# Performance work log

Measured on AMD Instinct MI355X. Metric: run time of the kernel, lower is better.

The kernel has to match this reference:

```python
import jax, jax.numpy as jnp
import numpy as np

D = 1024
H = 16
DH = D // H  # 64
EPS_LN = 1e-5
CONF_MIN = 1e-6


def sparsemax(z):
    """Sparsemax along the last axis (Martins & Astudillo 2016)."""
    K = z.shape[-1]
    z_sorted = jnp.flip(jnp.sort(z, axis=-1), axis=-1)          # descending
    cssv = jnp.cumsum(z_sorted, axis=-1)                        # cumulative sums
    r = jnp.arange(1, K + 1, dtype=z.dtype)                     # 1..K
    support = (1.0 + r * z_sorted) > cssv                       # bool mask
    k = jnp.sum(support, axis=-1, keepdims=True)                # support size
    tau = (jnp.take_along_axis(cssv, k.astype(jnp.int32) - 1, axis=-1) - 1.0) / k.astype(z.dtype)
    return jnp.maximum(z - tau, 0.0)


def setup_inputs() -> dict:
    key = jax.random.key(0)
    ks = jax.random.split(key, 16)
    B, P, K = 8, 512, 16
    s = 0.02
    return {
        "cell_query": jax.random.normal(ks[0], (B, D), jnp.float32),
        "gene_facets": jax.random.normal(ks[1], (B, P, K, D), jnp.float32),
        "confidence": jax.random.uniform(ks[2], (B, P, K), jnp.float32),
        "wq": jax.random.normal(ks[3], (D, D), jnp.float32) * s,
        "bq": jnp.zeros((D,), jnp.float32),
        "wk": jax.random.normal(ks[4], (D, D), jnp.float32) * s,
        "bk": jnp.zeros((D,), jnp.float32),
        "wv": jax.random.normal(ks[5], (D, D), jnp.float32) * s,
        "bv": jnp.zeros((D,), jnp.float32),
        "wo": jax.random.normal(ks[6], (D, D), jnp.float32) * s,
        "bo": jnp.zeros((D,), jnp.float32),
        "gamma": jnp.ones((D,), jnp.float32),
        "beta": jnp.zeros((D,), jnp.float32),
    }


def reference(cell_query, gene_facets, confidence,
              wq, bq, wk, bk, wv, bv, wo, bo, gamma, beta):
    B = gene_facets.shape[0]
    P = gene_facets.shape[1]
    Kf = gene_facets.shape[2]

    # Projections (torch Linear: x @ W^T + b; here weights stored already transposed as (D,D))
    Q = (cell_query @ wq + bq).reshape(B, H, DH)                       # (B,H,d)
    Kp = (gene_facets @ wk + bk).reshape(B, P, Kf, H, DH)              # (B,P,K,H,d)
    Vp = (gene_facets @ wv + bv).reshape(B, P, Kf, H, DH)              # (B,P,K,H,d)

    # scores: (B,P,H,K)
    scores = jnp.einsum('bhd,bpkhd->bphk', Q, Kp) / jnp.sqrt(jnp.asarray(DH, Q.dtype))
    conf_bias = jnp.log(jnp.clip(confidence, CONF_MIN))                # (B,P,K)
    scores = scores + conf_bias[:, :, None, :]

    alpha = sparsemax(scores)                                          # (B,P,H,K), dropout_p=0 -> identity

    out = jnp.einsum('bphk,bpkhd->bphd', alpha, Vp).reshape(B, P, D)
    out = out @ wo + bo

    # LayerNorm over last dim
    mu = jnp.mean(out, axis=-1, keepdims=True)
    var = jnp.mean((out - mu) ** 2, axis=-1, keepdims=True)
    out = (out - mu) * jax.lax.rsqrt(var + EPS_LN) * gamma + beta
    return out, alpha
```

## Files before the change

kernel.cpp:

```cpp
#include <hip/hip_runtime.h>


typedef float f32x4 __attribute__((ext_vector_type(4)));
typedef short s16x4 __attribute__((ext_vector_type(4)));
typedef short s16x8 __attribute__((ext_vector_type(8)));

__device__ __forceinline__ unsigned short f2bf(float f) {
  unsigned u = __builtin_bit_cast(unsigned, f);
  u = (u + 0x7FFFu + ((u >> 16) & 1u)) >> 16;
  return (unsigned short)u;
}

__device__ __forceinline__ float bf2f(unsigned short u) {
  return __builtin_bit_cast(float, ((unsigned)u) << 16);
}

__device__ __forceinline__ s16x8 pack8(s16x4 lo, s16x4 hi) {
  s16x8 r;
  r[0] = lo[0]; r[1] = lo[1]; r[2] = lo[2]; r[3] = lo[3];
  r[4] = hi[0]; r[5] = hi[1]; r[6] = hi[2]; r[7] = hi[3];
  return r;
}

__global__ __launch_bounds__(256) void k_transq(
    const float* __restrict__ wv, const float* __restrict__ wo,
    unsigned short* __restrict__ wvt, unsigned short* __restrict__ wot,
    const float* __restrict__ cq, const float* __restrict__ wq,
    float* __restrict__ qpart) {
  int bid = blockIdx.x;
  int t = threadIdx.x;
  if (bid < 512) {
    __shared__ float ts[64][65];
    const float* src = (bid < 256) ? wv : wo;
    unsigned short* dst = (bid < 256) ? wvt : wot;
    int tile = bid & 255;
    int er = (tile >> 4) << 6;
    int cb = (tile & 15) << 6;
    int r = t >> 2, c0 = (t & 3) << 4;
#pragma unroll
    for (int j = 0; j < 16; j += 4) {
      f32x4 v = *(const f32x4*)&src[(long)(er + r) * 1024 + cb + c0 + j];
      ts[r][c0 + j + 0] = v[0];
      ts[r][c0 + j + 1] = v[1];
      ts[r][c0 + j + 2] = v[2];
      ts[r][c0 + j + 3] = v[3];
    }
    __syncthreads();
    s16x8 o0, o1;
#pragma unroll
    for (int j = 0; j < 8; ++j) o0[j] = (short)f2bf(ts[c0 + j][r]);
#pragma unroll
    for (int j = 0; j < 8; ++j) o1[j] = (short)f2bf(ts[c0 + 8 + j][r]);
    long ob = (long)(cb + r) * 1024 + er + c0;
    *(s16x8*)&dst[ob] = o0;
    *(s16x8*)&dst[ob + 8] = o1;
  } else {
    int idx = bid - 512;
    int eq = idx >> 2, dq = idx & 3;
    int d = (dq << 8) + t;
    float acc[8] = {};
    for (int i = 0; i < 64; ++i) {
      int e = (eq << 6) + i;
      float w = wq[(long)e * 1024 + d];
#pragma unroll
      for (int b = 0; b < 8; ++b) acc[b] += w * cq[(b << 10) + e];
    }
#pragma unroll
    for (int b = 0; b < 8; ++b)
      qpart[(long)((b << 4) + eq) * 1024 + d] = acc[b];
  }
}

__global__ __launch_bounds__(256) void k_wtilde(
    const float* __restrict__ wk, const float* __restrict__ bk,
    const float* __restrict__ bq, const float* __restrict__ qpart,
    unsigned short* __restrict__ wt, float* __restrict__ cvec) {
  __shared__ float Qs[16][68];
  int et = blockIdx.x, b = blockIdx.y, t = threadIdx.x;
  {
    int d0 = t << 2;
    f32x4 s4 = *(const f32x4*)&bq[d0];
#pragma unroll
    for (int q = 0; q < 16; ++q)
      s4 += *(const f32x4*)&qpart[(long)((b << 4) + q) * 1024 + d0];
    *(f32x4*)&Qs[d0 >> 6][d0 & 63] = s4;
  }
  __syncthreads();
  int h = t & 15, el = t >> 4;
#pragma unroll
  for (int ii = 0; ii < 2; ++ii) {
    int e = (et << 5) + (ii << 4) + el;
    const float* wr = &wk[(long)e * 1024 + (h << 6)];
    float s = 0.f;
#pragma unroll
    for (int d = 0; d < 64; d += 4) {
      f32x4 w = *(const f32x4*)&wr[d];
      s += w[0] * Qs[h][d] + w[1] * Qs[h][d + 1] + w[2] * Qs[h][d + 2] + w[3] * Qs[h][d + 3];
    }
    wt[(long)((b << 4) + h) * 1024 + e] = f2bf(s);
  }
  if (et == 0 && t < 16) {
    float s = 0.f;
    for (int d = 0; d < 64; ++d) s += bk[(t << 6) + d] * Qs[t][d];
    cvec[(b << 4) + t] = s;
  }
}

#define GSTR 1028
#define TSTR 20
__global__ __launch_bounds__(256, 2) void k_scores(
    const float* __restrict__ G, const float* __restrict__ conf,
    const unsigned short* __restrict__ wt, const float* __restrict__ cvec,
    float* __restrict__ alpha_out, unsigned short* __restrict__ gbar,
    int b0, int hstride) {
  __shared__ short Gs[16 * GSTR];
  __shared__ short Gt[1024 * TSTR];
  __shared__ short As[16 * 32];
  __shared__ float ps[1024];
  __shared__ float lc[16];

  int t = threadIdx.x;
  int lane = t & 63, w = t >> 6;
  int l15 = lane & 15, g4 = lane >> 4;
  int bp = blockIdx.x;
  long gbp = (long)b0 * 512 + bp;
  int b = (int)(gbp >> 9);
  const float* Grow = G + gbp * 16384;
  const unsigned short* wtb = wt + (long)b * 16384;

#pragma unroll
  for (int half = 0; half < 2; ++half) {
    s16x4 col[8];
#pragma unroll
    for (int j = 0; j < 8; ++j) {
      int k = (half << 3) + j;
      f32x4 g = *(const f32x4*)&Grow[(k << 10) + (t << 2)];
      s16x4 h4;
      h4[0] = (short)f2bf(g[0]); h4[1] = (short)f2bf(g[1]);
      h4[2] = (short)f2bf(g[2]); h4[3] = (short)f2bf(g[3]);
      *(s16x4*)&Gs[k * GSTR + (t << 2)] = h4;
      col[j] = h4;
    }
#pragma unroll
    for (int q = 0; q < 4; ++q) {
      int e = (t << 2) + q;
      s16x4 lo, hi;
      lo[0] = col[0][q]; lo[1] = col[1][q]; lo[2] = col[2][q]; lo[3] = col[3][q];
      hi[0] = col[4][q]; hi[1] = col[5][q]; hi[2] = col[6][q]; hi[3] = col[7][q];
      *(s16x4*)&Gt[e * TSTR + (half << 3)] = lo;
      *(s16x4*)&Gt[e * TSTR + (half << 3) + 4] = hi;
    }
  }
  if (t < 16) lc[t] = logf(fmaxf(conf[gbp * 16 + t], 1e-6f));
  __syncthreads();

  f32x4 sc = {0.f, 0.f, 0.f, 0.f};
#pragma unroll
  for (int i = 0; i < 8; ++i) {
    int e0 = (w << 8) + (i << 5) + (g4 << 3);
    s16x8 af = *(const s16x8*)&wtb[l15 * 1024 + e0];
    int off = l15 * GSTR + e0;
    s16x8 bf = pack8(*(const s16x4*)&Gs[off], *(const s16x4*)&Gs[off + 4]);
    sc = __builtin_amdgcn_mfma_f32_16x16x32_bf16(af, bf, sc, 0, 0, 0);
  }
#pragma unroll
  for (int r = 0; r < 4; ++r)
    ps[(w << 8) + ((g4 << 2) + r) * 16 + l15] = sc[r];
  __syncthreads();

  {
    int h = t >> 4, k = t & 15;
    float z = (ps[h * 16 + k] + ps[256 + h * 16 + k] + ps[512 + h * 16 + k] +
               ps[768 + h * 16 + k] + cvec[b * 16 + h]) * 0.125f + lc[k];
    float v = z;
#pragma unroll
    for (int kk = 2; kk <= 16; kk <<= 1) {
#pragma unroll
      for (int j = kk >> 1; j > 0; j >>= 1) {
        float o = __shfl_xor(v, j, 64);
        bool dirDesc = ((l15 & kk) == 0);
        bool takeMax = (((l15 & j) == 0) == dirDesc);
        v = takeMax ? fmaxf(v, o) : fminf(v, o);
      }
    }
    float cs = v;
#pragma unroll
    for (int d = 1; d < 16; d <<= 1) {
      float o = __shfl_up(cs, (unsigned)d, 16);
      if (l15 >= d) cs += o;
    }
    bool sup = (1.0f + (float)(l15 + 1) * v) > cs;
    unsigned long long m = __ballot(sup);
    int gb16 = lane & 48;
    int ksup = (int)__popcll((m >> gb16) & 0xFFFFull);
    float csk = __shfl(cs, ksup - 1, 16);
    float tau = (csk - 1.0f) / (float)ksup;
    float a = fmaxf(z - tau, 0.0f);
    alpha_out[((gbp << 4) + h) * 16 + k] = a;
    As[(h << 5) + k] = (short)f2bf(a);
    As[(h << 5) + 16 + k] = 0;
  }
  __syncthreads();

  s16x8 ab = *(const s16x8*)&As[(l15 << 5) + (g4 << 3)];
#pragma unroll 4
  for (int i = 0; i < 16; ++i) {
    int ebase = ((w << 4) + i) << 4;
    int ro = (ebase + l15) * TSTR + ((g4 & 1) << 3);
    s16x8 aa = pack8(*(const s16x4*)&Gt[ro], *(const s16x4*)&Gt[ro + 4]);
    f32x4 d2 = __builtin_amdgcn_mfma_f32_16x16x32_bf16(
        aa, ab, (f32x4){0.f, 0.f, 0.f, 0.f}, 0, 0, 0);
    s16x4 o4;
    o4[0] = (short)f2bf(d2[0]); o4[1] = (short)f2bf(d2[1]);
    o4[2] = (short)f2bf(d2[2]); o4[3] = (short)f2bf(d2[3]);
    *(s16x4*)&Gs[l15 * GSTR + ebase + (g4 << 2)] = o4;
  }
  __syncthreads();

  unsigned short* gbo = gbar + (long)bp * 1024;
#pragma unroll
  for (int c2 = 0; c2 < 8; ++c2) {
    int flat = (c2 << 11) + (t << 3);
    int hh = flat >> 10, e = flat & 1023;
    s16x4 lo = *(const s16x4*)&Gs[hh * GSTR + e];
    s16x4 hi = *(const s16x4*)&Gs[hh * GSTR + e + 4];
    *(s16x8*)&gbo[(long)hh * hstride + e] = pack8(lo, hi);
  }
}

__global__ __launch_bounds__(256) void k_av(
    const unsigned short* __restrict__ gbar, const unsigned short* __restrict__ wvt,
    const float* __restrict__ bv, unsigned short* __restrict__ av,
    int b0, int hstride) {
  __shared__ short Asm[32 * 40];
  __shared__ short Bsm[64 * 40];
  int t = threadIdx.x;
  int lane = t & 63, w = t >> 6;
  int l15 = lane & 15, g4 = lane >> 4;
  int wm = w >> 1, wn = w & 1;
  int tile = blockIdx.x, h = blockIdx.y;
  const unsigned short* Ab = gbar + (long)h * hstride + (long)tile * 32 * 1024;
  const unsigned short* Bb = wvt + (long)(h << 6) * 1024;
  int ar = t >> 3, ac = (t & 7) << 2;
  int br = t >> 2, bc = (t & 3) << 3;
  const unsigned short* Arp = Ab + (long)ar * 1024 + ac;
  const unsigned short* Brp = Bb + (long)br * 1024 + bc;
  s16x4 a4 = *(const s16x4*)&Arp[0];
  s16x8 b8 = *(const s16x8*)&Brp[0];
  f32x4 acc[2] = {};
  for (int kb = 0; kb < 32; ++kb) {
    __syncthreads();
    *(s16x4*)&Asm[ar * 40 + ac] = a4;
    *(s16x8*)&Bsm[br * 40 + bc] = b8;
    if (kb + 1 < 32) {
      a4 = *(const s16x4*)&Arp[((kb + 1) << 5)];
      b8 = *(const s16x8*)&Brp[((kb + 1) << 5)];
    }
    __syncthreads();
    s16x8 afr = *(const s16x8*)&Asm[(wm * 16 + l15) * 40 + (g4 << 3)];
    s16x8 bfr[2];
#pragma unroll
    for (int in = 0; in < 2; ++in)
      bfr[in] = *(const s16x8*)&Bsm[(wn * 32 + in * 16 + l15) * 40 + (g4 << 3)];
#pragma unroll
    for (int in = 0; in < 2; ++in)
      acc[in] = __builtin_amdgcn_mfma_f32_16x16x32_bf16(afr, bfr[in], acc[in], 0, 0, 0);
  }
  long grow0 = (long)b0 * 512 + (long)tile * 32 + wm * 16 + (g4 << 2);
#pragma unroll
  for (int in = 0; in < 2; ++in) {
    int colg = (h << 6) + wn * 32 + in * 16 + l15;
    float bvv = bv[colg];
#pragma unroll
    for (int r = 0; r < 4; ++r)
      av[(grow0 + r) * 1024 + colg] = f2bf(acc[in][r] + bvv);
  }
}

__global__ __launch_bounds__(256) void k_out(
    const unsigned short* __restrict__ av, const unsigned short* __restrict__ wot,
    const float* __restrict__ bo, unsigned short* __restrict__ yb) {
  __shared__ short Asm[64 * 40];
  __shared__ short Bsm[64 * 40];
  int mt = blockIdx.x, nt = blockIdx.y, t = threadIdx.x;
  int lane = t & 63, w = t >> 6;
  int wm = w >> 1, wn = w & 1;
  int l15 = lane & 15, g4 = lane >> 4;
  int lr = t >> 2, lc = (t & 3) << 3;
  const unsigned short* Arp = av + (long)(mt * 64 + lr) * 1024 + lc;
  const unsigned short* Brp = wot + (long)(nt * 64 + lr) * 1024 + lc;
  s16x8 a8 = *(const s16x8*)&Arp[0];
  s16x8 b8 = *(const s16x8*)&Brp[0];
  f32x4 acc[2][2] = {};
  for (int kb = 0; kb < 32; ++kb) {
    __syncthreads();
    *(s16x8*)&Asm[lr * 40 + lc] = a8;
    *(s16x8*)&Bsm[lr * 40 + lc] = b8;
    if (kb + 1 < 32) {
      a8 = *(const s16x8*)&Arp[((kb + 1) << 5)];
      b8 = *(const s16x8*)&Brp[((kb + 1) << 5)];
    }
    __syncthreads();
    s16x8 afr[2], bfr[2];
#pragma unroll
    for (int im = 0; im < 2; ++im)
      afr[im] = *(const s16x8*)&Asm[(wm * 32 + im * 16 + l15) * 40 + (g4 << 3)];
#pragma unroll
    for (int in = 0; in < 2; ++in)
      bfr[in] = *(const s16x8*)&Bsm[(wn * 32 + in * 16 + l15) * 40 + (g4 << 3)];
#pragma unroll
    for (int im = 0; im < 2; ++im)
#pragma unroll
      for (int in = 0; in < 2; ++in)
        acc[im][in] = __builtin_amdgcn_mfma_f32_16x16x32_bf16(afr[im], bfr[in], acc[im][in], 0, 0, 0);
  }
#pragma unroll
  for (int in = 0; in < 2; ++in) {
    int colg = nt * 64 + wn * 32 + in * 16 + l15;
    float bov = bo[colg];
#pragma unroll
    for (int im = 0; im < 2; ++im) {
      long rowg = (long)mt * 64 + wm * 32 + im * 16 + (g4 << 2);
#pragma unroll
      for (int r = 0; r < 4; ++r)
        yb[(rowg + r) * 1024 + colg] = f2bf(acc[im][in][r] + bov);
    }
  }
}

__global__ __launch_bounds__(256) void k_ln(
    const unsigned short* __restrict__ yb, const float* __restrict__ gamma,
    const float* __restrict__ beta, float* __restrict__ y) {
  int row = (blockIdx.x << 2) + (threadIdx.x >> 6);
  int lane = threadIdx.x & 63;
  const unsigned short* yr = yb + ((long)row << 10);
  float v[4][4];
  float s = 0.f, s2 = 0.f;
#pragma unroll
  for (int j = 0; j < 4; ++j) {
    s16x4 h4 = *(const s16x4*)&yr[(lane << 2) + (j << 8)];
#pragma unroll
    for (int q = 0; q < 4; ++q) {
      float f = bf2f((unsigned short)h4[q]);
      v[j][q] = f; s += f; s2 += f * f;
    }
  }
#pragma unroll
  for (int d = 1; d < 64; d <<= 1) {
    s += __shfl_xor(s, d, 64);
    s2 += __shfl_xor(s2, d, 64);
  }
  float mu = s * (1.0f / 1024.0f);
  float var = s2 * (1.0f / 1024.0f) - mu * mu;
  float rs = rsqrtf(var + 1e-5f);
  float* yo = y + ((long)row << 10);
#pragma unroll
  for (int j = 0; j < 4; ++j) {
    int f0 = (lane << 2) + (j << 8);
    f32x4 gm = *(const f32x4*)&gamma[f0];
    f32x4 bt = *(const f32x4*)&beta[f0];
    f32x4 o;
#pragma unroll
    for (int q = 0; q < 4; ++q) o[q] = (v[j][q] - mu) * rs * gm[q] + bt[q];
    *(f32x4*)&yo[f0] = o;
  }
}

extern "C" void kernel_launch(void* const* d_in, const int* in_sizes, int n_in,
                              void* d_out, int out_size, void* d_ws, size_t ws_size,
                              hipStream_t stream) {
  (void)in_sizes; (void)n_in; (void)out_size;
  const float* cq    = (const float*)d_in[0];
  const float* G     = (const float*)d_in[1];
  const float* conf  = (const float*)d_in[2];
  const float* wq    = (const float*)d_in[3];
  const float* bq    = (const float*)d_in[4];
  const float* wk    = (const float*)d_in[5];
  const float* bk    = (const float*)d_in[6];
  const float* wv    = (const float*)d_in[7];
  const float* bv    = (const float*)d_in[8];
  const float* wo    = (const float*)d_in[9];
  const float* bo    = (const float*)d_in[10];
  const float* gamma = (const float*)d_in[11];
  const float* beta  = (const float*)d_in[12];

  float* y = (float*)d_out;
  float* alpha = y + 4194304;

  char* p = (char*)d_ws;
  float* qpart = (float*)p;                  p += 8L * 16 * 1024 * 4;
  float* cvec  = (float*)p;                  p += 1024;
  unsigned short* wt   = (unsigned short*)p; p += 8L * 16 * 1024 * 2;
  unsigned short* wvt  = (unsigned short*)p; p += 1024L * 1024 * 2;
  unsigned short* wot  = (unsigned short*)p; p += 1024L * 1024 * 2;
  unsigned short* av   = (unsigned short*)p; p += 4096L * 1024 * 2;
  unsigned short* yb   = (unsigned short*)p; p += 4096L * 1024 * 2;
  unsigned short* gbar = (unsigned short*)p;
  size_t used = (size_t)(p - (char*)d_ws);
  size_t per_b = 512L * 16 * 1024 * 2;
  int nb = 1;
  if (ws_size >= used + 4 * per_b) nb = 4;
  else if (ws_size >= used + 2 * per_b) nb = 2;
  int hstride = nb * 512 * 1024;

  hipLaunchKernelGGL(k_transq, dim3(576), dim3(256), 0, stream,
                     wv, wo, wvt, wot, cq, wq, qpart);
  hipLaunchKernelGGL(k_wtilde, dim3(32, 8), dim3(256), 0, stream, wk, bk, bq, qpart, wt, cvec);
  for (int c = 0; c < 8; c += nb) {
    hipLaunchKernelGGL(k_scores, dim3(nb * 512), dim3(256), 0, stream,
                       G, conf, wt, cvec, alpha, gbar, c, hstride);
    hipLaunchKernelGGL(k_av, dim3(nb * 16, 16), dim3(256), 0, stream,
                       gbar, wvt, bv, av, c, hstride);
  }
  hipLaunchKernelGGL(k_out, dim3(64, 16), dim3(256), 0, stream, av, wot, bo, yb);
  hipLaunchKernelGGL(k_ln, dim3(1024), dim3(256), 0, stream, yb, gamma, beta, y);
}
```

Baseline: 188.3 us.

## Fuse scores and AV kernels into one launch with double-buffered software pipeline

Merges k_scores and k_av into a single kernel in which the first blocks of the grid compute the AV GEMM for the previous batch chunk while the rest compute scores for the current chunk. The gbar intermediate is double-buffered so the two stages can overlap across launches. It also remaps k_out's block index so tiles are grouped per XCD, which should improve L2 reuse. This removes the tail and serialization between the two stages, at the cost of more launches on the fallback path and a larger shared-memory footprint for the AV blocks.

```diff
diff --git a/kernel.cpp b/kernel.cpp
--- a/kernel.cpp
+++ b/kernel.cpp
@@ -108,13 +108,14 @@
 
 #define GSTR 1028
 #define TSTR 20
-__global__ __launch_bounds__(256, 2) void k_scores(
+__global__ __launch_bounds__(256, 2) void k_scoav(
     const float* __restrict__ G, const float* __restrict__ conf,
     const unsigned short* __restrict__ wt, const float* __restrict__ cvec,
-    float* __restrict__ alpha_out, unsigned short* __restrict__ gbar,
-    int b0, int hstride) {
-  __shared__ short Gs[16 * GSTR];
-  __shared__ short Gt[1024 * TSTR];
+    float* __restrict__ alpha_out, unsigned short* __restrict__ gbw, int b0s,
+    const unsigned short* __restrict__ gbr, const unsigned short* __restrict__ wvt,
+    const float* __restrict__ bv, unsigned short* __restrict__ av, int b0a,
+    int nAv, int hstride) {
+  __shared__ short smem[16 * GSTR + 1024 * TSTR];
   __shared__ short As[16 * 32];
   __shared__ float ps[1024];
   __shared__ float lc[16];
@@ -122,8 +123,56 @@
   int t = threadIdx.x;
   int lane = t & 63, w = t >> 6;
   int l15 = lane & 15, g4 = lane >> 4;
-  int bp = blockIdx.x;
-  long gbp = (long)b0 * 512 + bp;
+
+  if ((int)blockIdx.x < nAv) {
+    short* Asm = smem;
+    short* Bsm = smem + 32 * 40;
+    int bid = blockIdx.x;
+    int tile = bid & 31, h = bid >> 5;
+    int wm = w >> 1, wn = w & 1;
+    const unsigned short* Ab = gbr + (long)h * hstride + (long)tile * 32 * 1024;
+    const unsigned short* Bb = wvt + (long)(h << 6) * 1024;
+    int ar = t >> 3, ac = (t & 7) << 2;
+    int br = t >> 2, bc = (t & 3) << 3;
+    const unsigned short* Arp = Ab + (long)ar * 1024 + ac;
+    const unsigned short* Brp = Bb + (long)br * 1024 + bc;
+    s16x4 a4 = *(const s16x4*)&Arp[0];
+    s16x8 b8 = *(const s16x8*)&Brp[0];
+    f32x4 acc[2] = {};
+    for (int kb = 0; kb < 32; ++kb) {
+      __syncthreads();
+      *(s16x4*)&Asm[ar * 40 + ac] = a4;
+      *(s16x8*)&Bsm[br * 40 + bc] = b8;
+      if (kb + 1 < 32) {
+        a4 = *(const s16x4*)&Arp[((kb + 1) << 5)];
+        b8 = *(const s16x8*)&Brp[((kb + 1) << 5)];
+      }
+      __syncthreads();
+      s16x8 afr = *(const s16x8*)&Asm[(wm * 16 + l15) * 40 + (g4 << 3)];
+      s16x8 bfr[2];
+#pragma unroll
+      for (int in = 0; in < 2; ++in)
+        bfr[in] = *(const s16x8*)&Bsm[(wn * 32 + in * 16 + l15) * 40 + (g4 << 3)];
+#pragma unroll
+      for (int in = 0; in < 2; ++in)
+        acc[in] = __builtin_amdgcn_mfma_f32_16x16x32_bf16(afr, bfr[in], acc[in], 0, 0, 0);
+    }
+    long grow0 = (long)b0a * 512 + (long)tile * 32 + wm * 16 + (g4 << 2);
+#pragma unroll
+    for (int in = 0; in < 2; ++in) {
+      int colg = (h << 6) + wn * 32 + in * 16 + l15;
+      float bvv = bv[colg];
+#pragma unroll
+      for (int r = 0; r < 4; ++r)
+        av[(grow0 + r) * 1024 + colg] = f2bf(acc[in][r] + bvv);
+    }
+    return;
+  }
+
+  short* Gs = smem;
+  short* Gt = smem + 16 * GSTR;
+  int bp = (int)blockIdx.x - nAv;
+  long gbp = (long)b0s * 512 + bp;
   int b = (int)(gbp >> 9);
   const float* Grow = G + gbp * 16384;
   const unsigned short* wtb = wt + (long)b * 16384;
@@ -217,7 +266,7 @@
   }
   __syncthreads();
 
-  unsigned short* gbo = gbar + (long)bp * 1024;
+  unsigned short* gbo = gbw + (long)bp * 1024;
 #pragma unroll
   for (int c2 = 0; c2 < 8; ++c2) {
     int flat = (c2 << 11) + (t << 3);
@@ -228,61 +277,16 @@
   }
 }
 
-__global__ __launch_bounds__(256) void k_av(
-    const unsigned short* __restrict__ gbar, const unsigned short* __restrict__ wvt,
-    const float* __restrict__ bv, unsigned short* __restrict__ av,
-    int b0, int hstride) {
-  __shared__ short Asm[32 * 40];
-  __shared__ short Bsm[64 * 40];
-  int t = threadIdx.x;
-  int lane = t & 63, w = t >> 6;
-  int l15 = lane & 15, g4 = lane >> 4;
-  int wm = w >> 1, wn = w & 1;
-  int tile = blockIdx.x, h = blockIdx.y;
-  const unsigned short* Ab = gbar + (long)h * hstride + (long)tile * 32 * 1024;
-  const unsigned short* Bb = wvt + (long)(h << 6) * 1024;
-  int ar = t >> 3, ac = (t & 7) << 2;
-  int br = t >> 2, bc = (t & 3) << 3;
-  const unsigned short* Arp = Ab + (long)ar * 1024 + ac;
-  const unsigned short* Brp = Bb + (long)br * 1024 + bc;
-  s16x4 a4 = *(const s16x4*)&Arp[0];
-  s16x8 b8 = *(const s16x8*)&Brp[0];
-  f32x4 acc[2] = {};
-  for (int kb = 0; kb < 32; ++kb) {
-    __syncthreads();
-    *(s16x4*)&Asm[ar * 40 + ac] = a4;
-    *(s16x8*)&Bsm[br * 40 + bc] = b8;
-    if (kb + 1 < 32) {
-      a4 = *(const s16x4*)&Arp[((kb + 1) << 5)];
-      b8 = *(const s16x8*)&Brp[((kb + 1) << 5)];
-    }
-    __syncthreads();
-    s16x8 afr = *(const s16x8*)&Asm[(wm * 16 + l15) * 40 + (g4 << 3)];
-    s16x8 bfr[2];
-#pragma unroll
-    for (int in = 0; in < 2; ++in)
-      bfr[in] = *(const s16x8*)&Bsm[(wn * 32 + in * 16 + l15) * 40 + (g4 << 3)];
-#pragma unroll
-    for (int in = 0; in < 2; ++in)
-      acc[in] = __builtin_amdgcn_mfma_f32_16x16x32_bf16(afr, bfr[in], acc[in], 0, 0, 0);
-  }
-  long grow0 = (long)b0 * 512 + (long)tile * 32 + wm * 16 + (g4 << 2);
-#pragma unroll
-  for (int in = 0; in < 2; ++in) {
-    int colg = (h << 6) + wn * 32 + in * 16 + l15;
-    float bvv = bv[colg];
-#pragma unroll
-    for (int r = 0; r < 4; ++r)
-      av[(grow0 + r) * 1024 + colg] = f2bf(acc[in][r] + bvv);
-  }
-}
-
 __global__ __launch_bounds__(256) void k_out(
     const unsigned short* __restrict__ av, const unsigned short* __restrict__ wot,
     const float* __restrict__ bo, unsigned short* __restrict__ yb) {
+  int bid = blockIdx.x;
+  int xcd = bid & 7, idx = bid >> 3;
+  int mt = ((xcd & 3) << 4) + (idx & 15);
+  int nt = ((xcd >> 2) << 3) + (idx >> 4);
   __shared__ short Asm[64 * 40];
   __shared__ short Bsm[64 * 40];
-  int mt = blockIdx.x, nt = blockIdx.y, t = threadIdx.x;
+  int t = threadIdx.x;
   int lane = t & 63, w = t >> 6;
   int wm = w >> 1, wn = w & 1;
   int l15 = lane & 15, g4 = lane >> 4;
@@ -395,23 +399,41 @@
   unsigned short* wot  = (unsigned short*)p; p += 1024L * 1024 * 2;
   unsigned short* av   = (unsigned short*)p; p += 4096L * 1024 * 2;
   unsigned short* yb   = (unsigned short*)p; p += 4096L * 1024 * 2;
-  unsigned short* gbar = (unsigned short*)p;
+  unsigned short* gbarA = (unsigned short*)p;
   size_t used = (size_t)(p - (char*)d_ws);
-  size_t per_b = 512L * 16 * 1024 * 2;
-  int nb = 1;
-  if (ws_size >= used + 4 * per_b) nb = 4;
-  else if (ws_size >= used + 2 * per_b) nb = 2;
-  int hstride = nb * 512 * 1024;
+  const int hstride = 2 * 512 * 1024;
+  size_t buf_bytes = 16L * hstride * 2;
+  unsigned short* gbarB = gbarA + 16L * hstride;
+  bool dual = (ws_size >= used + 2 * buf_bytes);
 
   hipLaunchKernelGGL(k_transq, dim3(576), dim3(256), 0, stream,
                      wv, wo, wvt, wot, cq, wq, qpart);
   hipLaunchKernelGGL(k_wtilde, dim3(32, 8), dim3(256), 0, stream, wk, bk, bq, qpart, wt, cvec);
-  for (int c = 0; c < 8; c += nb) {
-    hipLaunchKernelGGL(k_scores, dim3(nb * 512), dim3(256), 0, stream,
-                       G, conf, wt, cvec, alpha, gbar, c, hstride);
-    hipLaunchKernelGGL(k_av, dim3(nb * 16, 16), dim3(256), 0, stream,
-                       gbar, wvt, bv, av, c, hstride);
-  }
-  hipLaunchKernelGGL(k_out, dim3(64, 16), dim3(256), 0, stream, av, wot, bo, yb);
+
+  if (dual) {
+    unsigned short* bufs[2] = {gbarA, gbarB};
+    hipLaunchKernelGGL(k_scoav, dim3(1024), dim3(256), 0, stream,
+                       G, conf, wt, cvec, alpha, bufs[0], 0,
+                       bufs[0], wvt, bv, av, 0, 0, hstride);
+    for (int i = 1; i < 4; ++i) {
+      hipLaunchKernelGGL(k_scoav, dim3(1536), dim3(256), 0, stream,
+                         G, conf, wt, cvec, alpha, bufs[i & 1], i * 2,
+                         bufs[(i - 1) & 1], wvt, bv, av, (i - 1) * 2, 512, hstride);
+    }
+    hipLaunchKernelGGL(k_scoav, dim3(512), dim3(256), 0, stream,
+                       G, conf, wt, cvec, alpha, bufs[1], 0,
+                       bufs[1], wvt, bv, av, 6, 512, hstride);
+  } else {
+    for (int c = 0; c < 8; c += 2) {
+      hipLaunchKernelGGL(k_scoav, dim3(1024), dim3(256), 0, stream,
+                         G, conf, wt, cvec, alpha, gbarA, c,
+                         gbarA, wvt, bv, av, 0, 0, hstride);
+      hipLaunchKernelGGL(k_scoav, dim3(512), dim3(256), 0, stream,
+                         G, conf, wt, cvec, alpha, gbarA, 0,
+                         gbarA, wvt, bv, av, c, 512, hstride);
+    }
+  }
+
+  hipLaunchKernelGGL(k_out, dim3(1024), dim3(256), 0, stream, av, wot, bo, yb);
   hipLaunchKernelGGL(k_ln, dim3(1024), dim3(256), 0, stream, yb, gamma, beta, y);
 }
```

After: 206.7 us. 9.8% more time.
